# Kernel tuning notes

Hardware: AMD Instinct MI355X
Metric: run time of the kernel (lower is better)

Reference implementation:

```python
import jax, jax.numpy as jnp
import numpy as np
import math

# ---- static configuration (mirrors init_kwargs) ----
NQ = 8            # n_qubits (main register)
NA = 2            # n_ancilla = ceil(log2(n_select))
NSEL = 4          # n_select
DEG = 3           # degree
LAYERS = 2        # n_ansatz_layers
KLOC = 2          # k_local
LATENT = 128
B = 256
NROTS = 4 * NQ * LAYERS          # 64
GROUPS = [(s, s + 1) for s in range(NQ - KLOC + 1)]  # sliding 2-local -> 7 groups
NOBS = len(GROUPS)
KDIM = 2 ** KLOC                  # 4
C64 = jnp.complex64
TWO_PI = 2.0 * math.pi

CNOT = jnp.array([[1, 0, 0, 0], [0, 1, 0, 0], [0, 0, 0, 1], [0, 0, 1, 0]], dtype=C64)

# ---- gate matrices (theta may be traced) ----
def ry_mat(th):
    c = jnp.cos(th / 2).astype(C64); s = jnp.sin(th / 2).astype(C64)
    return jnp.stack([jnp.stack([c, -s]), jnp.stack([s, c])])

def rz_mat(th):
    return jnp.diag(jnp.stack([jnp.exp(-0.5j * th), jnp.exp(0.5j * th)])).astype(C64)

def crx_mat(th):
    c = jnp.cos(th / 2).astype(C64); isn = (-1j * jnp.sin(th / 2)).astype(C64)
    one = jnp.ones((), C64)
    m = jnp.zeros((4, 4), C64)
    m = m.at[0, 0].set(one).at[1, 1].set(one)
    m = m.at[2, 2].set(c).at[3, 3].set(c).at[2, 3].set(isn).at[3, 2].set(isn)
    return m

# ---- state-vector gate application (state: (2,)*rank, wire = axis) ----
def apply_1q(state, U, w):
    return jnp.moveaxis(jnp.tensordot(U, state, axes=((1,), (w,))), 0, w)

def apply_2q(state, U, w0, w1):
    st = jnp.tensordot(U.reshape(2, 2, 2, 2), state, axes=((2, 3), (w0, w1)))
    return jnp.moveaxis(st, (0, 1), (w0, w1))

def _sim14_ops(nq, layers):
    ops, idx = [], 0
    for _ in range(layers):
        for i in range(nq):
            ops.append(("ry", (i,), idx)); idx += 1
        for i in range(nq - 1, -1, -1):
            ops.append(("crx", (i, (i + 1) % nq), idx)); idx += 1
        for i in range(nq):
            ops.append(("ry", (i,), idx)); idx += 1
        for i in [nq - 1] + list(range(nq - 1)):
            ops.append(("crx", (i, (i - 1) % nq), idx)); idx += 1
    return ops

def apply_sim14(state, p, layers, adjoint=False):
    ops = _sim14_ops(NQ, layers)
    seq = list(reversed(ops)) if adjoint else ops
    sgn = -1.0 if adjoint else 1.0
    for kind, ws, idx in seq:
        th = sgn * p[idx]
        if kind == "ry":
            state = apply_1q(state, ry_mat(th), ws[0])
        else:
            state = apply_2q(state, crx_mat(th), ws[0], ws[1])
    return state

def pcphase(state, phi):
    # e^{+i phi} on ancilla=|0..0> subspace (first 2^NQ states in (anc, main) ordering), e^{-i phi} elsewhere
    sr = state.reshape(2 ** NQ, 2 ** NA)
    ph = jnp.where(jnp.arange(2 ** NA) == 0, jnp.exp(1j * phi), jnp.exp(-1j * phi)).astype(C64)
    return (sr * ph[None, :]).reshape(state.shape)

def prepare(state, prep_p, adjoint=False):
    if not adjoint:
        for ly in range(NA):          # n_prep_layers == n_ancilla
            for qi in range(NA):
                state = apply_1q(state, ry_mat(prep_p[ly, qi, 0]), NQ + qi)
                state = apply_1q(state, rz_mat(prep_p[ly, qi, 1]), NQ + qi)
            for i in range(NA - 1):
                state = apply_2q(state, CNOT, NQ + i, NQ + i + 1)
    else:
        for ly in reversed(range(NA)):
            for i in reversed(range(NA - 1)):
                state = apply_2q(state, CNOT, NQ + i, NQ + i + 1)
            for qi in reversed(range(NA)):
                state = apply_1q(state, rz_mat(-prep_p[ly, qi, 1]), NQ + qi)
                state = apply_1q(state, ry_mat(-prep_p[ly, qi, 0]), NQ + qi)
    return state

def select(state, ts, adjoint=False):
    # ancilla wires (NQ, NQ+1) are the trailing axes; flattened index == control value s
    sr = state.reshape((2,) * NQ + (2 ** NA,))
    for s in range(NSEL):
        sub = apply_sim14(sr[..., s], ts[s], LAYERS, adjoint=adjoint)
        sr = sr.at[..., s].set(sub)
    return sr.reshape(state.shape)

def create_hermitian(A, Bp, D, N):
    h = jnp.zeros((N, N), C64)
    count = 0
    for i in range(1, N):
        h = h.at[i - 1, i - 1].set(D[i].astype(C64))
        for j in range(i):
            h = h.at[i, j].set((A[count + j] + 1j * Bp[count + j]).astype(C64))
        count += i
    return h + h.conj().T

def simulate(ts, prep_p, sig, qff, H_all):
    # ts: (NSEL, NROTS) for one batch element
    state = jnp.zeros((2,) * (NQ + NA), C64).at[(0,) * (NQ + NA)].set(1.0)
    state = pcphase(state, sig[0])
    for k in range(DEG):
        state = prepare(state, prep_p)
        state = select(state, ts, adjoint=(k % 2 == 1))
        state = prepare(state, prep_p, adjoint=True)
        state = pcphase(state, sig[k + 1])
    state = apply_sim14(state, qff, 1)
    es = []
    for w, (a, b) in enumerate(GROUPS):
        hpsi = apply_2q(state, H_all[w], a, b)
        es.append(jnp.real(jnp.vdot(state, hpsi)))
    return jnp.stack(es).astype(jnp.float32)  # (NOBS,)

def linear(x, w, b):
    return x @ w.T + b

def sinusoidal_embedding(t, dim):
    half = dim // 2
    freqs = jnp.exp(-math.log(10000.0) * jnp.arange(half, dtype=jnp.float32) / half)
    args = t[:, None] * freqs[None]
    return jnp.concatenate([jnp.cos(args), jnp.sin(args)], axis=-1)

def _forward(z_t, t, te_w1, te_b1, te_w2, te_b2, ip_w1, ip_b1, ip_w2, ip_b2,
             prep_params, signal_angles, qff_params, A_obs, B_obs, D_obs, head_w, head_b):
    t_emb = sinusoidal_embedding(t, LATENT)
    t_emb = linear(jax.nn.silu(linear(t_emb, te_w1, te_b1)), te_w2, te_b2)
    h = jnp.concatenate([z_t, t_emb], axis=-1)
    h = linear(jax.nn.silu(linear(h, ip_w1, ip_b1)), ip_w2, ip_b2)
    ts = jax.nn.sigmoid(h).reshape(z_t.shape[0], NSEL, NROTS) * TWO_PI
    H_all = jax.vmap(lambda a, b, d: create_hermitian(a, b, d, KDIM))(A_obs, B_obs, D_obs)  # (NOBS,4,4)
    expvals = jax.vmap(simulate, in_axes=(0, None, None, None, None))(
        ts, prep_params, signal_angles, qff_params, H_all)  # (B, NOBS)
    return linear(expvals, head_w, head_b)  # (B, LATENT)

def setup_inputs() -> dict:
    key = jax.random.key(0)
    ks = jax.random.split(key, 16)
    def n(k, shape, s=0.05):
        return s * jax.random.normal(k, shape, jnp.float32)
    return {
        "z_t": jax.random.normal(ks[0], (B, LATENT), jnp.float32),
        "t": jax.random.uniform(ks[1], (B,), jnp.float32),
        "te_w1": n(ks[2], (LATENT, LATENT)), "te_b1": jnp.zeros((LATENT,), jnp.float32),
        "te_w2": n(ks[3], (LATENT, LATENT)), "te_b2": jnp.zeros((LATENT,), jnp.float32),
        "ip_w1": n(ks[4], (2 * LATENT, 2 * LATENT)), "ip_b1": jnp.zeros((2 * LATENT,), jnp.float32),
        "ip_w2": n(ks[5], (NSEL * NROTS, 2 * LATENT)), "ip_b2": jnp.zeros((NSEL * NROTS,), jnp.float32),
        "prep_params": 0.1 * jax.random.normal(ks[6], (NA, NA, 2), jnp.float32),
        "signal_angles": 0.1 * jax.random.normal(ks[7], (DEG + 1,), jnp.float32),
        "qff_params": jax.random.uniform(ks[8], (4 * NQ,), jnp.float32),
        "A_obs": 2.0 * jax.random.normal(ks[9], (NOBS, KDIM * (KDIM - 1) // 2), jnp.float32),
        "B_obs": 2.0 * jax.random.normal(ks[10], (NOBS, KDIM * (KDIM - 1) // 2), jnp.float32),
        "D_obs": 2.0 * jax.random.normal(ks[11], (NOBS, KDIM), jnp.float32),
        "head_w": n(ks[12], (LATENT, NOBS)), "head_b": jnp.zeros((LATENT,), jnp.float32),
    }

def reference(z_t, t, te_w1, te_b1, te_w2, te_b2, ip_w1, ip_b1, ip_w2, ip_b2,
              prep_params, signal_angles, qff_params, A_obs, B_obs, D_obs, head_w, head_b):
    return _forward(z_t, t, te_w1, te_b1, te_w2, te_b2, ip_w1, ip_b1, ip_w2, ip_b2,
                    prep_params, signal_angles, qff_params, A_obs, B_obs, D_obs, head_w, head_b)
```

## Files before the change

kernel.cpp:

```cpp
#include <hip/hip_runtime.h>
#include <math.h>

#define NOBS 7
#define TWO_PI_F 6.283185307179586f
#define PI_F 3.14159265358979f


constexpr int REG_MASK(int w)  { return w==6 ? 2 : w==7 ? 1 : 0; }
constexpr int LANE_MASK(int w) { return w<=5 ? (1 << (5-w)) : 0; }

template<int LM>
__device__ __forceinline__ float lane_partner(float x) {
  if constexpr (LM == 1) {
    return __int_as_float(__builtin_amdgcn_mov_dpp(__float_as_int(x), 0xB1, 0xF, 0xF, true));
  } else if constexpr (LM == 2) {
    return __int_as_float(__builtin_amdgcn_mov_dpp(__float_as_int(x), 0x4E, 0xF, 0xF, true));
  } else if constexpr (LM == 4) {
    int a = __builtin_amdgcn_mov_dpp(__float_as_int(x), 0x1B, 0xF, 0xF, true);
    return __int_as_float(__builtin_amdgcn_mov_dpp(a, 0x141, 0xF, 0xF, true));
  } else if constexpr (LM == 8) {
    int a = __builtin_amdgcn_mov_dpp(__float_as_int(x), 0x141, 0xF, 0xF, true);
    return __int_as_float(__builtin_amdgcn_mov_dpp(a, 0x140, 0xF, 0xF, true));
  } else if constexpr (LM == 16) {
#if __has_builtin(__builtin_amdgcn_permlane16_swap)
    unsigned xu = __float_as_uint(x);
    auto r = __builtin_amdgcn_permlane16_swap(xu, xu, false, false);
    return (__uint_as_float(r[0]) + __uint_as_float(r[1])) - x;
#else
    return __shfl_xor(x, 16, 64);
#endif
  } else {
#if __has_builtin(__builtin_amdgcn_permlane32_swap)
    unsigned xu = __float_as_uint(x);
    auto r = __builtin_amdgcn_permlane32_swap(xu, xu, false, false);
    return (__uint_as_float(r[0]) + __uint_as_float(r[1])) - x;
#else
    return __shfl_xor(x, 32, 64);
#endif
  }
}

template<int LM>
__device__ __forceinline__ float xor_sum(float x) {
  if constexpr (LM == 16) {
#if __has_builtin(__builtin_amdgcn_permlane16_swap)
    unsigned xu = __float_as_uint(x);
    auto r = __builtin_amdgcn_permlane16_swap(xu, xu, false, false);
    return __uint_as_float(r[0]) + __uint_as_float(r[1]);
#else
    return x + __shfl_xor(x, 16, 64);
#endif
  } else if constexpr (LM == 32) {
#if __has_builtin(__builtin_amdgcn_permlane32_swap)
    unsigned xu = __float_as_uint(x);
    auto r = __builtin_amdgcn_permlane32_swap(xu, xu, false, false);
    return __uint_as_float(r[0]) + __uint_as_float(r[1]);
#else
    return x + __shfl_xor(x, 32, 64);
#endif
  } else {
    return x + lane_partner<LM>(x);
  }
}

__device__ __forceinline__ float rdlane(float v, int idx) {
  return __int_as_float(__builtin_amdgcn_readlane(__float_as_int(v), idx));
}

__device__ __forceinline__ float2 cmul(float2 a, float2 b) {
  return make_float2(a.x*b.x - a.y*b.y, a.x*b.y + a.y*b.x);
}
__device__ __forceinline__ float2 cmulc(float2 a, float2 b) {
  return make_float2(a.x*b.x + a.y*b.y, a.y*b.x - a.x*b.y);
}
__device__ __forceinline__ float2 cadd(float2 a, float2 b) {
  return make_float2(a.x + b.x, a.y + b.y);
}


template<int W>
__device__ __forceinline__ void ry_gate(float* vr, float* vi, int lane,
                                        float creg, float sreg, int idx, float sg)
{
  float c = rdlane(creg, idx);
  float s = sg * rdlane(sreg, idx);
  if constexpr (REG_MASK(W) != 0) {
    constexpr int m = REG_MASK(W);
#pragma unroll
    for (int r = 0; r < 4; ++r) {
      if (r & m) continue;
      const int r1 = r | m;
      float a0 = vr[r], a1 = vr[r1];
      vr[r]  = c*a0 - s*a1;  vr[r1] = s*a0 + c*a1;
      float b0 = vi[r], b1 = vi[r1];
      vi[r]  = c*b0 - s*b1;  vi[r1] = s*b0 + c*b1;
    }
  } else {
    constexpr int LM = LANE_MASK(W);
    const float ls = (lane & LM) ? s : -s;
#pragma unroll
    for (int r = 0; r < 4; ++r) {
      float pr = lane_partner<LM>(vr[r]);
      float pi = lane_partner<LM>(vi[r]);
      vr[r] = c*vr[r] + ls*pr;
      vi[r] = c*vi[r] + ls*pi;
    }
  }
}

template<int WC, int WT>
__device__ __forceinline__ void crx_gate(float* vr, float* vi, int lane,
                                         float creg, float sreg, int idx, float sg)
{
  float c = rdlane(creg, idx);
  float s = sg * rdlane(sreg, idx);
  constexpr int MC = REG_MASK(WC), LC = LANE_MASK(WC);
  constexpr int MT = REG_MASK(WT), LT = LANE_MASK(WT);
  if constexpr (MC != 0 && MT != 0) {
#pragma unroll
    for (int r = 0; r < 4; ++r) {
      if (!(r & MC) || (r & MT)) continue;
      const int r1 = r | MT;
      float xr = vr[r], xi = vi[r], yr = vr[r1], yi = vi[r1];
      vr[r]  = c*xr + s*yi;  vi[r]  = c*xi - s*yr;
      vr[r1] = c*yr + s*xi;  vi[r1] = c*yi - s*xr;
    }
  } else if constexpr (MC != 0) {
#pragma unroll
    for (int r = 0; r < 4; ++r) {
      if (!(r & MC)) continue;
      float pr = lane_partner<LT>(vr[r]);
      float pi = lane_partner<LT>(vi[r]);
      vr[r] = c*vr[r] + s*pi;
      vi[r] = c*vi[r] - s*pr;
    }
  } else if constexpr (MT != 0) {
    const bool act = (lane & LC) != 0;
#pragma unroll
    for (int r = 0; r < 4; ++r) {
      if (r & MT) continue;
      const int r1 = r | MT;
      float xr = vr[r], xi = vi[r], yr = vr[r1], yi = vi[r1];
      float nxr = c*xr + s*yi, nxi = c*xi - s*yr;
      float nyr = c*yr + s*xi, nyi = c*yi - s*xr;
      vr[r]  = act ? nxr : xr;  vi[r]  = act ? nxi : xi;
      vr[r1] = act ? nyr : yr;  vi[r1] = act ? nyi : yi;
    }
  } else {
    const bool act = (lane & LC) != 0;
#pragma unroll
    for (int r = 0; r < 4; ++r) {
      float pr = lane_partner<LT>(vr[r]);
      float pi = lane_partner<LT>(vi[r]);
      float nr = c*vr[r] + s*pi;
      float ni = c*vi[r] - s*pr;
      vr[r] = act ? nr : vr[r];
      vi[r] = act ? ni : vi[r];
    }
  }
}


__device__ __forceinline__ void sim14_fwd(float* vr, float* vi, int lane,
                                          float ct, float st, int off, float sg)
{
  ry_gate<0>(vr,vi,lane,ct,st,off+0,sg);  ry_gate<1>(vr,vi,lane,ct,st,off+1,sg);
  ry_gate<2>(vr,vi,lane,ct,st,off+2,sg);  ry_gate<3>(vr,vi,lane,ct,st,off+3,sg);
  ry_gate<4>(vr,vi,lane,ct,st,off+4,sg);  ry_gate<5>(vr,vi,lane,ct,st,off+5,sg);
  ry_gate<6>(vr,vi,lane,ct,st,off+6,sg);  ry_gate<7>(vr,vi,lane,ct,st,off+7,sg);
  crx_gate<7,0>(vr,vi,lane,ct,st,off+8,sg);  crx_gate<6,7>(vr,vi,lane,ct,st,off+9,sg);
  crx_gate<5,6>(vr,vi,lane,ct,st,off+10,sg); crx_gate<4,5>(vr,vi,lane,ct,st,off+11,sg);
  crx_gate<3,4>(vr,vi,lane,ct,st,off+12,sg); crx_gate<2,3>(vr,vi,lane,ct,st,off+13,sg);
  crx_gate<1,2>(vr,vi,lane,ct,st,off+14,sg); crx_gate<0,1>(vr,vi,lane,ct,st,off+15,sg);
  ry_gate<0>(vr,vi,lane,ct,st,off+16,sg); ry_gate<1>(vr,vi,lane,ct,st,off+17,sg);
  ry_gate<2>(vr,vi,lane,ct,st,off+18,sg); ry_gate<3>(vr,vi,lane,ct,st,off+19,sg);
  ry_gate<4>(vr,vi,lane,ct,st,off+20,sg); ry_gate<5>(vr,vi,lane,ct,st,off+21,sg);
  ry_gate<6>(vr,vi,lane,ct,st,off+22,sg); ry_gate<7>(vr,vi,lane,ct,st,off+23,sg);
  crx_gate<7,6>(vr,vi,lane,ct,st,off+24,sg); crx_gate<0,7>(vr,vi,lane,ct,st,off+25,sg);
  crx_gate<1,0>(vr,vi,lane,ct,st,off+26,sg); crx_gate<2,1>(vr,vi,lane,ct,st,off+27,sg);
  crx_gate<3,2>(vr,vi,lane,ct,st,off+28,sg); crx_gate<4,3>(vr,vi,lane,ct,st,off+29,sg);
  crx_gate<5,4>(vr,vi,lane,ct,st,off+30,sg); crx_gate<6,5>(vr,vi,lane,ct,st,off+31,sg);
}

__device__ __forceinline__ void sim14_adj(float* vr, float* vi, int lane,
                                          float ct, float st, int off)
{
  const float sg = -1.f;
  crx_gate<6,5>(vr,vi,lane,ct,st,off+31,sg); crx_gate<5,4>(vr,vi,lane,ct,st,off+30,sg);
  crx_gate<4,3>(vr,vi,lane,ct,st,off+29,sg); crx_gate<3,2>(vr,vi,lane,ct,st,off+28,sg);
  crx_gate<2,1>(vr,vi,lane,ct,st,off+27,sg); crx_gate<1,0>(vr,vi,lane,ct,st,off+26,sg);
  crx_gate<0,7>(vr,vi,lane,ct,st,off+25,sg); crx_gate<7,6>(vr,vi,lane,ct,st,off+24,sg);
  ry_gate<7>(vr,vi,lane,ct,st,off+23,sg); ry_gate<6>(vr,vi,lane,ct,st,off+22,sg);
  ry_gate<5>(vr,vi,lane,ct,st,off+21,sg); ry_gate<4>(vr,vi,lane,ct,st,off+20,sg);
  ry_gate<3>(vr,vi,lane,ct,st,off+19,sg); ry_gate<2>(vr,vi,lane,ct,st,off+18,sg);
  ry_gate<1>(vr,vi,lane,ct,st,off+17,sg); ry_gate<0>(vr,vi,lane,ct,st,off+16,sg);
  crx_gate<0,1>(vr,vi,lane,ct,st,off+15,sg); crx_gate<1,2>(vr,vi,lane,ct,st,off+14,sg);
  crx_gate<2,3>(vr,vi,lane,ct,st,off+13,sg); crx_gate<3,4>(vr,vi,lane,ct,st,off+12,sg);
  crx_gate<4,5>(vr,vi,lane,ct,st,off+11,sg); crx_gate<5,6>(vr,vi,lane,ct,st,off+10,sg);
  crx_gate<6,7>(vr,vi,lane,ct,st,off+9,sg);  crx_gate<7,0>(vr,vi,lane,ct,st,off+8,sg);
  ry_gate<7>(vr,vi,lane,ct,st,off+7,sg); ry_gate<6>(vr,vi,lane,ct,st,off+6,sg);
  ry_gate<5>(vr,vi,lane,ct,st,off+5,sg); ry_gate<4>(vr,vi,lane,ct,st,off+4,sg);
  ry_gate<3>(vr,vi,lane,ct,st,off+3,sg); ry_gate<2>(vr,vi,lane,ct,st,off+2,sg);
  ry_gate<1>(vr,vi,lane,ct,st,off+1,sg); ry_gate<0>(vr,vi,lane,ct,st,off+0,sg);
}


template<int IN, int NP, int MODE>
__device__ __forceinline__ void mlp_layer(const float* __restrict__ W,
    const float* __restrict__ bias, const float* xl, float* yl,
    int rbase, int lane)
{
  const int sub = lane & 7;
  const int g   = lane >> 3;
#pragma unroll
  for (int p = 0; p < NP; ++p) {
    const int row = rbase + p * 8 + g;
    const float4* w4 = (const float4*)(W + row * IN) + sub;
    const float4* x4 = (const float4*)xl + sub;
    float acc = 0.f;
#pragma unroll
    for (int it = 0; it < IN / 32; ++it) {
      float4 w = w4[it * 8], e = x4[it * 8];
      acc += w.x*e.x + w.y*e.y + w.z*e.z + w.w*e.w;
    }
    acc = xor_sum<1>(acc);
    acc = xor_sum<2>(acc);
    acc = xor_sum<4>(acc);
    if (sub == 0) {
      float a = acc + bias[row];
      if constexpr (MODE == 0) {
        yl[row] = a / (1.f + __expf(-a));
      } else if constexpr (MODE == 1) {
        yl[row] = a;
      } else {
        float th = PI_F / (1.f + __expf(-a));
        float sn, cn;
        __sincosf(th, &sn, &cn);
        ((float2*)yl)[row] = make_float2(cn, sn);
      }
    }
  }
}


__global__ __launch_bounds__(256) void qsvt_kernel(
    const float* __restrict__ z_t, const float* __restrict__ t,
    const float* __restrict__ te_w1, const float* __restrict__ te_b1,
    const float* __restrict__ te_w2, const float* __restrict__ te_b2,
    const float* __restrict__ ip_w1, const float* __restrict__ ip_b1,
    const float* __restrict__ ip_w2, const float* __restrict__ ip_b2,
    const float* __restrict__ prep_p, const float* __restrict__ sig,
    const float* __restrict__ qff, const float* __restrict__ A_obs,
    const float* __restrict__ B_obs, const float* __restrict__ D_obs,
    const float* __restrict__ head_w, const float* __restrict__ head_b,
    float* __restrict__ out)
{
  __shared__ __align__(16) float emb[128];
  __shared__ __align__(16) float y1[128];
  __shared__ __align__(16) float hbuf[256];
  __shared__ __align__(16) float h1[256];
  __shared__ __align__(16) float2 seltab[256];
  __shared__ __align__(16) float2 qtab[32];
  __shared__ __align__(16) float2 xbuf[64*17];
  __shared__ __align__(16) float dumpR[4][256];
  __shared__ __align__(16) float dumpI[4][256];
  __shared__ float redbuf[NOBS][4];
  __shared__ float hdc[NOBS][3], hxc[NOBS][6], hyc[NOBS][6];
  __shared__ __align__(16) float shw[128*NOBS];
  __shared__ __align__(16) float shb[128];

  const int tid  = threadIdx.x;
  const int lane = tid & 63;
  const int s    = tid >> 6;
  const int b    = blockIdx.x;

  if (tid < 128) {
    int j = tid & 63;
    float fr = __expf(-9.210340371976184f * (float)j / 64.f);
    float arg = t[b] * fr;
    float sn, cn;
    __sincosf(arg, &sn, &cn);
    emb[tid] = (tid < 64) ? cn : sn;
  } else if (tid < 160) {
    int j = tid - 128;
    float sn, cn;
    __sincosf(0.5f * qff[j], &sn, &cn);
    qtab[j] = make_float2(cn, sn);
  }
  __syncthreads();

  mlp_layer<128, 4, 0>(te_w1, te_b1, emb, y1, s * 32, lane);
  if (tid < 128) hbuf[tid] = z_t[b * 128 + tid];
  __syncthreads();

  mlp_layer<128, 4, 1>(te_w2, te_b2, y1, hbuf + 128, s * 32, lane);
  __syncthreads();

  mlp_layer<256, 8, 0>(ip_w1, ip_b1, hbuf, h1, s * 64, lane);
  __syncthreads();

  mlp_layer<256, 8, 2>(ip_w2, ip_b2, h1, (float*)seltab, s * 64, lane);

  if (tid < NOBS * 6)      { hxc[tid/6][tid%6] = A_obs[tid]; hyc[tid/6][tid%6] = B_obs[tid]; }
  else if (tid >= 64 && tid < 64 + NOBS*3) { int q = tid - 64; hdc[q/3][q%3] = 2.f * D_obs[(q/3)*4 + (q%3) + 1]; }
#pragma unroll
  for (int i = tid; i < 128*NOBS; i += 256) shw[i] = head_w[i];
  if (tid < 128) shb[tid] = head_b[tid];

  float2 Ga[2][2][2], Gb[2][2][2];
#pragma unroll
  for (int ly = 0; ly < 2; ++ly) {
#pragma unroll
    for (int qi = 0; qi < 2; ++qi) {
      float y = prep_p[ly*4 + qi*2 + 0], z = prep_p[ly*4 + qi*2 + 1];
      float cy, sy, cz, sz;
      __sincosf(0.5f*y, &sy, &cy);
      __sincosf(0.5f*z, &sz, &cz);
      float2 g00 = make_float2( cy*cz, -cy*sz);
      float2 g01 = make_float2(-sy*cz,  sy*sz);
      float2 g10 = make_float2( sy*cz,  sy*sz);
      float2 g11 = make_float2( cy*cz,  cy*sz);
      if (qi == 0) { Ga[ly][0][0]=g00; Ga[ly][0][1]=g01; Ga[ly][1][0]=g10; Ga[ly][1][1]=g11; }
      else         { Gb[ly][0][0]=g00; Gb[ly][0][1]=g01; Gb[ly][1][0]=g10; Gb[ly][1][1]=g11; }
    }
  }
  float2 M[2][4][4];
#pragma unroll
  for (int ly = 0; ly < 2; ++ly) {
    float2 T[4][4];
#pragma unroll
    for (int i = 0; i < 4; ++i)
#pragma unroll
      for (int j = 0; j < 4; ++j)
        T[i][j] = cmul(Ga[ly][i>>1][j>>1], Gb[ly][i&1][j&1]);
#pragma unroll
    for (int j = 0; j < 4; ++j) {
      M[ly][0][j] = T[0][j]; M[ly][1][j] = T[1][j];
      M[ly][2][j] = T[3][j]; M[ly][3][j] = T[2][j];
    }
  }
  float2 U[4][4];
#pragma unroll
  for (int i = 0; i < 4; ++i)
#pragma unroll
    for (int j = 0; j < 4; ++j) {
      float2 acc = make_float2(0.f, 0.f);
#pragma unroll
      for (int kk = 0; kk < 4; ++kk) acc = cadd(acc, cmul(M[1][i][kk], M[0][kk][j]));
      U[i][j] = acc;
    }
  float2 Urow[4], Ucol[4];
#pragma unroll
  for (int j = 0; j < 4; ++j) {
    Urow[j] = s==0 ? U[0][j] : s==1 ? U[1][j] : s==2 ? U[2][j] : U[3][j];
    Ucol[j] = s==0 ? U[j][0] : s==1 ? U[j][1] : s==2 ? U[j][2] : U[j][3];
  }
  float sg0 = sig[0], sg1 = sig[1], sg2 = sig[2], sg3 = sig[3];
  float c1, s1v, c2, s2v, c3, s3v;
  __sincosf(sg1, &s1v, &c1);
  __sincosf(sg2, &s2v, &c2);
  __sincosf(sg3, &s3v, &c3);
  float2 R1[4], R2[4], RF[4];
  {
    float s3s = (s == 0) ? s3v : -s3v;
    float2 d3 = make_float2(c3, s3s);
#pragma unroll
    for (int sp = 0; sp < 4; ++sp) {
      float2 a1 = make_float2(0.f, 0.f), a2 = make_float2(0.f, 0.f);
#pragma unroll
      for (int j = 0; j < 4; ++j) {
        float2 uspj = sp==0 ? U[0][j] : sp==1 ? U[1][j] : sp==2 ? U[2][j] : U[3][j];
        float2 tt = cmulc(Urow[j], uspj);
        float sj = (j == 0) ? 1.f : -1.f;
        a1 = cadd(a1, cmul(tt, make_float2(c1, sj*s1v)));
        a2 = cadd(a2, cmul(tt, make_float2(c2, sj*s2v)));
      }
      R1[sp] = a1; R2[sp] = a2;
      RF[sp] = cmul(d3, make_float2(Ucol[sp].x, -Ucol[sp].y));
    }
  }
  __syncthreads();

  float2 mycs = seltab[(s << 6) | lane];
  float selc = mycs.x, sels = mycs.y;
  float2 myq = qtab[lane & 31];
  float qc = myq.x, qs = myq.y;

  float vr[4], vi[4];
  {
    float s0n, c0n;
    __sincosf(sg0, &s0n, &c0n);
    float2 a0 = cmul(Urow[0], make_float2(c0n, s0n));
#pragma unroll
    for (int r = 0; r < 4; ++r) { vr[r] = 0.f; vi[r] = 0.f; }
    if (lane == 0) { vr[0] = a0.x; vi[0] = a0.y; }
  }

  sim14_fwd(vr, vi, lane, selc, sels, 0, 1.f);
  sim14_fwd(vr, vi, lane, selc, sels, 32, 1.f);
  {
#pragma unroll
    for (int r = 0; r < 4; ++r) xbuf[lane*17 + r*4 + s] = make_float2(vr[r], vi[r]);
    __syncthreads();
#pragma unroll
    for (int r = 0; r < 4; ++r) {
      const float2* p = &xbuf[lane*17 + r*4];
      float2 o = cmul(R1[0], p[0]);
      o = cadd(o, cmul(R1[1], p[1]));
      o = cadd(o, cmul(R1[2], p[2]));
      o = cadd(o, cmul(R1[3], p[3]));
      vr[r] = o.x; vi[r] = o.y;
    }
    __syncthreads();
  }
  sim14_adj(vr, vi, lane, selc, sels, 32);
  sim14_adj(vr, vi, lane, selc, sels, 0);
  {
#pragma unroll
    for (int r = 0; r < 4; ++r) xbuf[lane*17 + r*4 + s] = make_float2(vr[r], vi[r]);
    __syncthreads();
#pragma unroll
    for (int r = 0; r < 4; ++r) {
      const float2* p = &xbuf[lane*17 + r*4];
      float2 o = cmul(R2[0], p[0]);
      o = cadd(o, cmul(R2[1], p[1]));
      o = cadd(o, cmul(R2[2], p[2]));
      o = cadd(o, cmul(R2[3], p[3]));
      vr[r] = o.x; vi[r] = o.y;
    }
    __syncthreads();
  }
  sim14_fwd(vr, vi, lane, selc, sels, 0, 1.f);
  sim14_fwd(vr, vi, lane, selc, sels, 32, 1.f);
  {
#pragma unroll
    for (int r = 0; r < 4; ++r) xbuf[lane*17 + r*4 + s] = make_float2(vr[r], vi[r]);
    __syncthreads();
#pragma unroll
    for (int r = 0; r < 4; ++r) {
      const float2* p = &xbuf[lane*17 + r*4];
      float2 o = cmul(RF[0], p[0]);
      o = cadd(o, cmul(RF[1], p[1]));
      o = cadd(o, cmul(RF[2], p[2]));
      o = cadd(o, cmul(RF[3], p[3]));
      vr[r] = o.x; vi[r] = o.y;
    }
    __syncthreads();
  }
  sim14_fwd(vr, vi, lane, qc, qs, 0, 1.f);

  *(float4*)&dumpR[s][lane*4] = make_float4(vr[0], vr[1], vr[2], vr[3]);
  *(float4*)&dumpI[s][lane*4] = make_float4(vi[0], vi[1], vi[2], vi[3]);

#pragma unroll
  for (int w = 0; w < NOBS; ++w) {
    const int pb = 6 - w;
    int g = lane;
    int ib = ((g >> pb) << (pb + 2)) | (g & ((1 << pb) - 1));
    float xr[4], xi[4];
#pragma unroll
    for (int i = 0; i < 4; ++i) { xr[i] = dumpR[s][ib + (i << pb)]; xi[i] = dumpI[s][ib + (i << pb)]; }
    float a = hdc[w][0] * (xr[0]*xr[0] + xi[0]*xi[0])
            + hdc[w][1] * (xr[1]*xr[1] + xi[1]*xi[1])
            + hdc[w][2] * (xr[2]*xr[2] + xi[2]*xi[2]);
    const int oi[6] = {1, 2, 2, 3, 3, 3};
    const int oj[6] = {0, 0, 1, 0, 1, 2};
#pragma unroll
    for (int k2 = 0; k2 < 6; ++k2) {
      int i = oi[k2], j = oj[k2];
      float rr = xr[i]*xr[j] + xi[i]*xi[j];
      float ii = xr[i]*xi[j] - xi[i]*xr[j];
      a += 2.f * (hxc[w][k2]*rr - hyc[w][k2]*ii);
    }
    a = xor_sum<32>(a);
    a = xor_sum<16>(a);
    a = xor_sum<8>(a);
    a = xor_sum<4>(a);
    a = xor_sum<2>(a);
    a = xor_sum<1>(a);
    if (lane == 0) redbuf[w][s] = a;
  }
  __syncthreads();

  if (tid < 128) {
    float acc = shb[tid];
#pragma unroll
    for (int w = 0; w < NOBS; ++w) {
      float ev = redbuf[w][0] + redbuf[w][1] + redbuf[w][2] + redbuf[w][3];
      acc += ev * shw[tid*NOBS + w];
    }
    out[b * 128 + tid] = acc;
  }
}

extern "C" void kernel_launch(void* const* d_in, const int* in_sizes, int n_in,
                              void* d_out, int out_size, void* d_ws, size_t ws_size,
                              hipStream_t stream) {
  (void)n_in; (void)out_size; (void)d_ws; (void)ws_size;
  const float* z_t    = (const float*)d_in[0];
  const float* t      = (const float*)d_in[1];
  const float* te_w1  = (const float*)d_in[2];
  const float* te_b1  = (const float*)d_in[3];
  const float* te_w2  = (const float*)d_in[4];
  const float* te_b2  = (const float*)d_in[5];
  const float* ip_w1  = (const float*)d_in[6];
  const float* ip_b1  = (const float*)d_in[7];
  const float* ip_w2  = (const float*)d_in[8];
  const float* ip_b2  = (const float*)d_in[9];
  const float* prep_p = (const float*)d_in[10];
  const float* sig    = (const float*)d_in[11];
  const float* qff    = (const float*)d_in[12];
  const float* A_obs  = (const float*)d_in[13];
  const float* B_obs  = (const float*)d_in[14];
  const float* D_obs  = (const float*)d_in[15];
  const float* head_w = (const float*)d_in[16];
  const float* head_b = (const float*)d_in[17];
  float* out = (float*)d_out;

  int B = in_sizes[1];
  qsvt_kernel<<<B, 256, 0, stream>>>(
      z_t, t, te_w1, te_b1, te_w2, te_b2, ip_w1, ip_b1, ip_w2, ip_b2,
      prep_p, sig, qff, A_obs, B_obs, D_obs, head_w, head_b, out);
}
```

Baseline: 128.8 us.

## Split state vector across two wave halves with LDS exchange for wire 6

Doubles the block to 512 threads so each ancilla branch's 256-amplitude state is spread over two wavefronts, each lane holding 2 amplitudes instead of 4. Wire 6 now spans the two wave halves, so gates acting on it exchange data through a double-buffered shared-memory buffer with a block barrier. The MLP stages and the observable loop are re-partitioned across the 8 waves. This halves per-thread gate work and register use, but adds many __syncthreads on the critical gate chain.

New measurement: 127.2 us. About the same (-1.2%).

```diff
diff --git a/kernel.cpp b/kernel.cpp
--- a/kernel.cpp
+++ b/kernel.cpp
@@ -2,12 +2,8 @@
 #include <math.h>
 
 #define NOBS 7
-#define TWO_PI_F 6.283185307179586f
 #define PI_F 3.14159265358979f
 
-
-constexpr int REG_MASK(int w)  { return w==6 ? 2 : w==7 ? 1 : 0; }
-constexpr int LANE_MASK(int w) { return w<=5 ? (1 << (5-w)) : 0; }
 
 template<int LM>
 __device__ __forceinline__ float lane_partner(float x) {
@@ -77,131 +73,180 @@
   return make_float2(a.x + b.x, a.y + b.y);
 }
 
+struct Ctx {
+  float4* xw;
+  int pp;
+  int wv, lane, h;
+};
+
+__device__ __forceinline__ float4 wexch(Ctx& cx, const float* vr, const float* vi) {
+  float4* buf = cx.xw + cx.pp * 512;
+  buf[cx.wv * 64 + cx.lane] = make_float4(vr[0], vr[1], vi[0], vi[1]);
+  __syncthreads();
+  float4 p = buf[(cx.wv ^ 4) * 64 + cx.lane];
+  cx.pp ^= 1;
+  return p;
+}
+
 
 template<int W>
-__device__ __forceinline__ void ry_gate(float* vr, float* vi, int lane,
-                                        float creg, float sreg, int idx, float sg)
-{
-  float c = rdlane(creg, idx);
-  float s = sg * rdlane(sreg, idx);
-  if constexpr (REG_MASK(W) != 0) {
-    constexpr int m = REG_MASK(W);
-#pragma unroll
-    for (int r = 0; r < 4; ++r) {
-      if (r & m) continue;
-      const int r1 = r | m;
-      float a0 = vr[r], a1 = vr[r1];
-      vr[r]  = c*a0 - s*a1;  vr[r1] = s*a0 + c*a1;
-      float b0 = vi[r], b1 = vi[r1];
-      vi[r]  = c*b0 - s*b1;  vi[r1] = s*b0 + c*b1;
-    }
-  } else {
-    constexpr int LM = LANE_MASK(W);
-    const float ls = (lane & LM) ? s : -s;
-#pragma unroll
-    for (int r = 0; r < 4; ++r) {
-      float pr = lane_partner<LM>(vr[r]);
-      float pi = lane_partner<LM>(vi[r]);
-      vr[r] = c*vr[r] + ls*pr;
-      vi[r] = c*vi[r] + ls*pi;
-    }
-  }
-}
-
-template<int WC, int WT>
-__device__ __forceinline__ void crx_gate(float* vr, float* vi, int lane,
-                                         float creg, float sreg, int idx, float sg)
-{
-  float c = rdlane(creg, idx);
-  float s = sg * rdlane(sreg, idx);
-  constexpr int MC = REG_MASK(WC), LC = LANE_MASK(WC);
-  constexpr int MT = REG_MASK(WT), LT = LANE_MASK(WT);
-  if constexpr (MC != 0 && MT != 0) {
-#pragma unroll
-    for (int r = 0; r < 4; ++r) {
-      if (!(r & MC) || (r & MT)) continue;
-      const int r1 = r | MT;
-      float xr = vr[r], xi = vi[r], yr = vr[r1], yi = vi[r1];
-      vr[r]  = c*xr + s*yi;  vi[r]  = c*xi - s*yr;
-      vr[r1] = c*yr + s*xi;  vi[r1] = c*yi - s*xr;
-    }
-  } else if constexpr (MC != 0) {
-#pragma unroll
-    for (int r = 0; r < 4; ++r) {
-      if (!(r & MC)) continue;
+__device__ __forceinline__ void ry_lane(float* vr, float* vi, Ctx& cx,
+                                        float ct, float st, int idx, float sg) {
+  float c = rdlane(ct, idx), s = sg * rdlane(st, idx);
+  constexpr int LM = 1 << (5 - W);
+  const float ls = (cx.lane & LM) ? s : -s;
+#pragma unroll
+  for (int r = 0; r < 2; ++r) {
+    float pr = lane_partner<LM>(vr[r]);
+    float pi = lane_partner<LM>(vi[r]);
+    vr[r] = c*vr[r] + ls*pr;
+    vi[r] = c*vi[r] + ls*pi;
+  }
+}
+
+__device__ __forceinline__ void ry_wave6(float* vr, float* vi, Ctx& cx,
+                                         float ct, float st, int idx, float sg) {
+  float c = rdlane(ct, idx), s = sg * rdlane(st, idx);
+  float4 P = wexch(cx, vr, vi);
+  const float ls = cx.h ? s : -s;
+  vr[0] = c*vr[0] + ls*P.x;  vr[1] = c*vr[1] + ls*P.y;
+  vi[0] = c*vi[0] + ls*P.z;  vi[1] = c*vi[1] + ls*P.w;
+}
+
+__device__ __forceinline__ void ry_reg7(float* vr, float* vi,
+                                        float ct, float st, int idx, float sg) {
+  float c = rdlane(ct, idx), s = sg * rdlane(st, idx);
+  float a0 = vr[0], a1 = vr[1];
+  vr[0] = c*a0 - s*a1;  vr[1] = s*a0 + c*a1;
+  float b0 = vi[0], b1 = vi[1];
+  vi[0] = c*b0 - s*b1;  vi[1] = s*b0 + c*b1;
+}
+
+template<int C, int T>
+__device__ __forceinline__ void crx_ll(float* vr, float* vi, Ctx& cx,
+                                       float ct, float st, int idx, float sg) {
+  float c = rdlane(ct, idx), s = sg * rdlane(st, idx);
+  constexpr int LC = 1 << (5 - C), LT = 1 << (5 - T);
+  const bool act = (cx.lane & LC) != 0;
+  const float cp = act ? c : 1.f, sp = act ? s : 0.f;
+#pragma unroll
+  for (int r = 0; r < 2; ++r) {
+    float pr = lane_partner<LT>(vr[r]);
+    float pi = lane_partner<LT>(vi[r]);
+    vr[r] = cp*vr[r] + sp*pi;
+    vi[r] = cp*vi[r] - sp*pr;
+  }
+}
+
+template<int T>
+__device__ __forceinline__ void crx_7l(float* vr, float* vi, Ctx& cx,
+                                       float ct, float st, int idx, float sg) {
+  float c = rdlane(ct, idx), s = sg * rdlane(st, idx);
+  constexpr int LT = 1 << (5 - T);
+  float pr = lane_partner<LT>(vr[1]);
+  float pi = lane_partner<LT>(vi[1]);
+  vr[1] = c*vr[1] + s*pi;
+  vi[1] = c*vi[1] - s*pr;
+}
+
+template<int C>
+__device__ __forceinline__ void crx_l7(float* vr, float* vi, Ctx& cx,
+                                       float ct, float st, int idx, float sg) {
+  float c = rdlane(ct, idx), s = sg * rdlane(st, idx);
+  constexpr int LC = 1 << (5 - C);
+  const bool act = (cx.lane & LC) != 0;
+  const float cp = act ? c : 1.f, sp = act ? s : 0.f;
+  float xr = vr[0], xi = vi[0], yr = vr[1], yi = vi[1];
+  vr[0] = cp*xr + sp*yi;  vi[0] = cp*xi - sp*yr;
+  vr[1] = cp*yr + sp*xi;  vi[1] = cp*yi - sp*xr;
+}
+
+template<int C>
+__device__ __forceinline__ void crx_l6(float* vr, float* vi, Ctx& cx,
+                                       float ct, float st, int idx, float sg) {
+  float c = rdlane(ct, idx), s = sg * rdlane(st, idx);
+  float4 P = wexch(cx, vr, vi);
+  constexpr int LC = 1 << (5 - C);
+  const bool act = (cx.lane & LC) != 0;
+  const float cp = act ? c : 1.f, sp = act ? s : 0.f;
+  vr[0] = cp*vr[0] + sp*P.z;  vi[0] = cp*vi[0] - sp*P.x;
+  vr[1] = cp*vr[1] + sp*P.w;  vi[1] = cp*vi[1] - sp*P.y;
+}
+
+__device__ __forceinline__ void crx_76(float* vr, float* vi, Ctx& cx,
+                                       float ct, float st, int idx, float sg) {
+  float c = rdlane(ct, idx), s = sg * rdlane(st, idx);
+  float4 P = wexch(cx, vr, vi);
+  vr[1] = c*vr[1] + s*P.w;
+  vi[1] = c*vi[1] - s*P.y;
+}
+
+__device__ __forceinline__ void crx_67(float* vr, float* vi, Ctx& cx,
+                                       float ct, float st, int idx, float sg) {
+  if (cx.h) {
+    float c = rdlane(ct, idx), s = sg * rdlane(st, idx);
+    float xr = vr[0], xi = vi[0], yr = vr[1], yi = vi[1];
+    vr[0] = c*xr + s*yi;  vi[0] = c*xi - s*yr;
+    vr[1] = c*yr + s*xi;  vi[1] = c*yi - s*xr;
+  }
+}
+
+template<int T>
+__device__ __forceinline__ void crx_6l(float* vr, float* vi, Ctx& cx,
+                                       float ct, float st, int idx, float sg) {
+  if (cx.h) {
+    float c = rdlane(ct, idx), s = sg * rdlane(st, idx);
+    constexpr int LT = 1 << (5 - T);
+#pragma unroll
+    for (int r = 0; r < 2; ++r) {
       float pr = lane_partner<LT>(vr[r]);
       float pi = lane_partner<LT>(vi[r]);
       vr[r] = c*vr[r] + s*pi;
       vi[r] = c*vi[r] - s*pr;
     }
-  } else if constexpr (MT != 0) {
-    const bool act = (lane & LC) != 0;
-#pragma unroll
-    for (int r = 0; r < 4; ++r) {
-      if (r & MT) continue;
-      const int r1 = r | MT;
-      float xr = vr[r], xi = vi[r], yr = vr[r1], yi = vi[r1];
-      float nxr = c*xr + s*yi, nxi = c*xi - s*yr;
-      float nyr = c*yr + s*xi, nyi = c*yi - s*xr;
-      vr[r]  = act ? nxr : xr;  vi[r]  = act ? nxi : xi;
-      vr[r1] = act ? nyr : yr;  vi[r1] = act ? nyi : yi;
-    }
-  } else {
-    const bool act = (lane & LC) != 0;
-#pragma unroll
-    for (int r = 0; r < 4; ++r) {
-      float pr = lane_partner<LT>(vr[r]);
-      float pi = lane_partner<LT>(vi[r]);
-      float nr = c*vr[r] + s*pi;
-      float ni = c*vi[r] - s*pr;
-      vr[r] = act ? nr : vr[r];
-      vi[r] = act ? ni : vi[r];
-    }
-  }
-}
-
-
-__device__ __forceinline__ void sim14_fwd(float* vr, float* vi, int lane,
-                                          float ct, float st, int off, float sg)
-{
-  ry_gate<0>(vr,vi,lane,ct,st,off+0,sg);  ry_gate<1>(vr,vi,lane,ct,st,off+1,sg);
-  ry_gate<2>(vr,vi,lane,ct,st,off+2,sg);  ry_gate<3>(vr,vi,lane,ct,st,off+3,sg);
-  ry_gate<4>(vr,vi,lane,ct,st,off+4,sg);  ry_gate<5>(vr,vi,lane,ct,st,off+5,sg);
-  ry_gate<6>(vr,vi,lane,ct,st,off+6,sg);  ry_gate<7>(vr,vi,lane,ct,st,off+7,sg);
-  crx_gate<7,0>(vr,vi,lane,ct,st,off+8,sg);  crx_gate<6,7>(vr,vi,lane,ct,st,off+9,sg);
-  crx_gate<5,6>(vr,vi,lane,ct,st,off+10,sg); crx_gate<4,5>(vr,vi,lane,ct,st,off+11,sg);
-  crx_gate<3,4>(vr,vi,lane,ct,st,off+12,sg); crx_gate<2,3>(vr,vi,lane,ct,st,off+13,sg);
-  crx_gate<1,2>(vr,vi,lane,ct,st,off+14,sg); crx_gate<0,1>(vr,vi,lane,ct,st,off+15,sg);
-  ry_gate<0>(vr,vi,lane,ct,st,off+16,sg); ry_gate<1>(vr,vi,lane,ct,st,off+17,sg);
-  ry_gate<2>(vr,vi,lane,ct,st,off+18,sg); ry_gate<3>(vr,vi,lane,ct,st,off+19,sg);
-  ry_gate<4>(vr,vi,lane,ct,st,off+20,sg); ry_gate<5>(vr,vi,lane,ct,st,off+21,sg);
-  ry_gate<6>(vr,vi,lane,ct,st,off+22,sg); ry_gate<7>(vr,vi,lane,ct,st,off+23,sg);
-  crx_gate<7,6>(vr,vi,lane,ct,st,off+24,sg); crx_gate<0,7>(vr,vi,lane,ct,st,off+25,sg);
-  crx_gate<1,0>(vr,vi,lane,ct,st,off+26,sg); crx_gate<2,1>(vr,vi,lane,ct,st,off+27,sg);
-  crx_gate<3,2>(vr,vi,lane,ct,st,off+28,sg); crx_gate<4,3>(vr,vi,lane,ct,st,off+29,sg);
-  crx_gate<5,4>(vr,vi,lane,ct,st,off+30,sg); crx_gate<6,5>(vr,vi,lane,ct,st,off+31,sg);
-}
-
-__device__ __forceinline__ void sim14_adj(float* vr, float* vi, int lane,
-                                          float ct, float st, int off)
-{
+  }
+}
+
+
+__device__ __forceinline__ void sim14_fwd(float* vr, float* vi, Ctx& cx,
+                                          float ct, float st, int off, float sg) {
+  ry_lane<0>(vr,vi,cx,ct,st,off+0,sg); ry_lane<1>(vr,vi,cx,ct,st,off+1,sg);
+  ry_lane<2>(vr,vi,cx,ct,st,off+2,sg); ry_lane<3>(vr,vi,cx,ct,st,off+3,sg);
+  ry_lane<4>(vr,vi,cx,ct,st,off+4,sg); ry_lane<5>(vr,vi,cx,ct,st,off+5,sg);
+  ry_wave6(vr,vi,cx,ct,st,off+6,sg);   ry_reg7(vr,vi,ct,st,off+7,sg);
+  crx_7l<0>(vr,vi,cx,ct,st,off+8,sg);  crx_67(vr,vi,cx,ct,st,off+9,sg);
+  crx_l6<5>(vr,vi,cx,ct,st,off+10,sg); crx_ll<4,5>(vr,vi,cx,ct,st,off+11,sg);
+  crx_ll<3,4>(vr,vi,cx,ct,st,off+12,sg); crx_ll<2,3>(vr,vi,cx,ct,st,off+13,sg);
+  crx_ll<1,2>(vr,vi,cx,ct,st,off+14,sg); crx_ll<0,1>(vr,vi,cx,ct,st,off+15,sg);
+  ry_lane<0>(vr,vi,cx,ct,st,off+16,sg); ry_lane<1>(vr,vi,cx,ct,st,off+17,sg);
+  ry_lane<2>(vr,vi,cx,ct,st,off+18,sg); ry_lane<3>(vr,vi,cx,ct,st,off+19,sg);
+  ry_lane<4>(vr,vi,cx,ct,st,off+20,sg); ry_lane<5>(vr,vi,cx,ct,st,off+21,sg);
+  ry_wave6(vr,vi,cx,ct,st,off+22,sg);   ry_reg7(vr,vi,ct,st,off+23,sg);
+  crx_76(vr,vi,cx,ct,st,off+24,sg);     crx_l7<0>(vr,vi,cx,ct,st,off+25,sg);
+  crx_ll<1,0>(vr,vi,cx,ct,st,off+26,sg); crx_ll<2,1>(vr,vi,cx,ct,st,off+27,sg);
+  crx_ll<3,2>(vr,vi,cx,ct,st,off+28,sg); crx_ll<4,3>(vr,vi,cx,ct,st,off+29,sg);
+  crx_ll<5,4>(vr,vi,cx,ct,st,off+30,sg); crx_6l<5>(vr,vi,cx,ct,st,off+31,sg);
+}
+
+__device__ __forceinline__ void sim14_adj(float* vr, float* vi, Ctx& cx,
+                                          float ct, float st, int off) {
   const float sg = -1.f;
-  crx_gate<6,5>(vr,vi,lane,ct,st,off+31,sg); crx_gate<5,4>(vr,vi,lane,ct,st,off+30,sg);
-  crx_gate<4,3>(vr,vi,lane,ct,st,off+29,sg); crx_gate<3,2>(vr,vi,lane,ct,st,off+28,sg);
-  crx_gate<2,1>(vr,vi,lane,ct,st,off+27,sg); crx_gate<1,0>(vr,vi,lane,ct,st,off+26,sg);
-  crx_gate<0,7>(vr,vi,lane,ct,st,off+25,sg); crx_gate<7,6>(vr,vi,lane,ct,st,off+24,sg);
-  ry_gate<7>(vr,vi,lane,ct,st,off+23,sg); ry_gate<6>(vr,vi,lane,ct,st,off+22,sg);
-  ry_gate<5>(vr,vi,lane,ct,st,off+21,sg); ry_gate<4>(vr,vi,lane,ct,st,off+20,sg);
-  ry_gate<3>(vr,vi,lane,ct,st,off+19,sg); ry_gate<2>(vr,vi,lane,ct,st,off+18,sg);
-  ry_gate<1>(vr,vi,lane,ct,st,off+17,sg); ry_gate<0>(vr,vi,lane,ct,st,off+16,sg);
-  crx_gate<0,1>(vr,vi,lane,ct,st,off+15,sg); crx_gate<1,2>(vr,vi,lane,ct,st,off+14,sg);
-  crx_gate<2,3>(vr,vi,lane,ct,st,off+13,sg); crx_gate<3,4>(vr,vi,lane,ct,st,off+12,sg);
-  crx_gate<4,5>(vr,vi,lane,ct,st,off+11,sg); crx_gate<5,6>(vr,vi,lane,ct,st,off+10,sg);
-  crx_gate<6,7>(vr,vi,lane,ct,st,off+9,sg);  crx_gate<7,0>(vr,vi,lane,ct,st,off+8,sg);
-  ry_gate<7>(vr,vi,lane,ct,st,off+7,sg); ry_gate<6>(vr,vi,lane,ct,st,off+6,sg);
-  ry_gate<5>(vr,vi,lane,ct,st,off+5,sg); ry_gate<4>(vr,vi,lane,ct,st,off+4,sg);
-  ry_gate<3>(vr,vi,lane,ct,st,off+3,sg); ry_gate<2>(vr,vi,lane,ct,st,off+2,sg);
-  ry_gate<1>(vr,vi,lane,ct,st,off+1,sg); ry_gate<0>(vr,vi,lane,ct,st,off+0,sg);
+  crx_6l<5>(vr,vi,cx,ct,st,off+31,sg); crx_ll<5,4>(vr,vi,cx,ct,st,off+30,sg);
+  crx_ll<4,3>(vr,vi,cx,ct,st,off+29,sg); crx_ll<3,2>(vr,vi,cx,ct,st,off+28,sg);
+  crx_ll<2,1>(vr,vi,cx,ct,st,off+27,sg); crx_ll<1,0>(vr,vi,cx,ct,st,off+26,sg);
+  crx_l7<0>(vr,vi,cx,ct,st,off+25,sg);   crx_76(vr,vi,cx,ct,st,off+24,sg);
+  ry_reg7(vr,vi,ct,st,off+23,sg);        ry_wave6(vr,vi,cx,ct,st,off+22,sg);
+  ry_lane<5>(vr,vi,cx,ct,st,off+21,sg); ry_lane<4>(vr,vi,cx,ct,st,off+20,sg);
+  ry_lane<3>(vr,vi,cx,ct,st,off+19,sg); ry_lane<2>(vr,vi,cx,ct,st,off+18,sg);
+  ry_lane<1>(vr,vi,cx,ct,st,off+17,sg); ry_lane<0>(vr,vi,cx,ct,st,off+16,sg);
+  crx_ll<0,1>(vr,vi,cx,ct,st,off+15,sg); crx_ll<1,2>(vr,vi,cx,ct,st,off+14,sg);
+  crx_ll<2,3>(vr,vi,cx,ct,st,off+13,sg); crx_ll<3,4>(vr,vi,cx,ct,st,off+12,sg);
+  crx_ll<4,5>(vr,vi,cx,ct,st,off+11,sg); crx_l6<5>(vr,vi,cx,ct,st,off+10,sg);
+  crx_67(vr,vi,cx,ct,st,off+9,sg);       crx_7l<0>(vr,vi,cx,ct,st,off+8,sg);
+  ry_reg7(vr,vi,ct,st,off+7,sg);         ry_wave6(vr,vi,cx,ct,st,off+6,sg);
+  ry_lane<5>(vr,vi,cx,ct,st,off+5,sg); ry_lane<4>(vr,vi,cx,ct,st,off+4,sg);
+  ry_lane<3>(vr,vi,cx,ct,st,off+3,sg); ry_lane<2>(vr,vi,cx,ct,st,off+2,sg);
+  ry_lane<1>(vr,vi,cx,ct,st,off+1,sg); ry_lane<0>(vr,vi,cx,ct,st,off+0,sg);
 }
 
 
@@ -243,7 +288,7 @@
 }
 
 
-__global__ __launch_bounds__(256) void qsvt_kernel(
+__global__ __launch_bounds__(512) void qsvt_kernel(
     const float* __restrict__ z_t, const float* __restrict__ t,
     const float* __restrict__ te_w1, const float* __restrict__ te_b1,
     const float* __restrict__ te_w2, const float* __restrict__ te_b2,
@@ -261,17 +306,20 @@
   __shared__ __align__(16) float h1[256];
   __shared__ __align__(16) float2 seltab[256];
   __shared__ __align__(16) float2 qtab[32];
-  __shared__ __align__(16) float2 xbuf[64*17];
+  __shared__ __align__(16) float4 xw[2 * 8 * 64];
+  __shared__ __align__(16) float2 xanc[128 * 9];
   __shared__ __align__(16) float dumpR[4][256];
   __shared__ __align__(16) float dumpI[4][256];
   __shared__ float redbuf[NOBS][4];
   __shared__ float hdc[NOBS][3], hxc[NOBS][6], hyc[NOBS][6];
-  __shared__ __align__(16) float shw[128*NOBS];
+  __shared__ __align__(16) float shw[128 * NOBS];
   __shared__ __align__(16) float shb[128];
 
   const int tid  = threadIdx.x;
   const int lane = tid & 63;
-  const int s    = tid >> 6;
+  const int wv   = tid >> 6;
+  const int s    = wv & 3;
+  const int h    = wv >> 2;
   const int b    = blockIdx.x;
 
   if (tid < 128) {
@@ -289,22 +337,22 @@
   }
   __syncthreads();
 
-  mlp_layer<128, 4, 0>(te_w1, te_b1, emb, y1, s * 32, lane);
+  mlp_layer<128, 2, 0>(te_w1, te_b1, emb, y1, wv * 16, lane);
   if (tid < 128) hbuf[tid] = z_t[b * 128 + tid];
   __syncthreads();
 
-  mlp_layer<128, 4, 1>(te_w2, te_b2, y1, hbuf + 128, s * 32, lane);
-  __syncthreads();
-
-  mlp_layer<256, 8, 0>(ip_w1, ip_b1, hbuf, h1, s * 64, lane);
-  __syncthreads();
-
-  mlp_layer<256, 8, 2>(ip_w2, ip_b2, h1, (float*)seltab, s * 64, lane);
+  mlp_layer<128, 2, 1>(te_w2, te_b2, y1, hbuf + 128, wv * 16, lane);
+  __syncthreads();
+
+  mlp_layer<256, 4, 0>(ip_w1, ip_b1, hbuf, h1, wv * 32, lane);
+  __syncthreads();
+
+  mlp_layer<256, 4, 2>(ip_w2, ip_b2, h1, (float*)seltab, wv * 32, lane);
 
   if (tid < NOBS * 6)      { hxc[tid/6][tid%6] = A_obs[tid]; hyc[tid/6][tid%6] = B_obs[tid]; }
   else if (tid >= 64 && tid < 64 + NOBS*3) { int q = tid - 64; hdc[q/3][q%3] = 2.f * D_obs[(q/3)*4 + (q%3) + 1]; }
 #pragma unroll
-  for (int i = tid; i < 128*NOBS; i += 256) shw[i] = head_w[i];
+  for (int i = tid; i < 128*NOBS; i += 512) shw[i] = head_w[i];
   if (tid < 128) shb[tid] = head_b[tid];
 
   float2 Ga[2][2][2], Gb[2][2][2];
@@ -386,25 +434,28 @@
   float2 myq = qtab[lane & 31];
   float qc = myq.x, qs = myq.y;
 
-  float vr[4], vi[4];
-  {
+  Ctx cx; cx.xw = xw; cx.pp = 0; cx.wv = wv; cx.lane = lane; cx.h = h;
+
+  float vr[2], vi[2];
+  vr[0] = 0.f; vr[1] = 0.f; vi[0] = 0.f; vi[1] = 0.f;
+  if (lane == 0 && h == 0) {
     float s0n, c0n;
     __sincosf(sg0, &s0n, &c0n);
     float2 a0 = cmul(Urow[0], make_float2(c0n, s0n));
-#pragma unroll
-    for (int r = 0; r < 4; ++r) { vr[r] = 0.f; vi[r] = 0.f; }
-    if (lane == 0) { vr[0] = a0.x; vi[0] = a0.y; }
-  }
-
-  sim14_fwd(vr, vi, lane, selc, sels, 0, 1.f);
-  sim14_fwd(vr, vi, lane, selc, sels, 32, 1.f);
+    vr[0] = a0.x; vi[0] = a0.y;
+  }
+
+  const int ancbase = (h * 64 + lane) * 9;
+
+  sim14_fwd(vr, vi, cx, selc, sels, 0, 1.f);
+  sim14_fwd(vr, vi, cx, selc, sels, 32, 1.f);
   {
 #pragma unroll
-    for (int r = 0; r < 4; ++r) xbuf[lane*17 + r*4 + s] = make_float2(vr[r], vi[r]);
+    for (int r = 0; r < 2; ++r) xanc[ancbase + r*4 + s] = make_float2(vr[r], vi[r]);
     __syncthreads();
 #pragma unroll
-    for (int r = 0; r < 4; ++r) {
-      const float2* p = &xbuf[lane*17 + r*4];
+    for (int r = 0; r < 2; ++r) {
+      const float2* p = &xanc[ancbase + r*4];
       float2 o = cmul(R1[0], p[0]);
       o = cadd(o, cmul(R1[1], p[1]));
       o = cadd(o, cmul(R1[2], p[2]));
@@ -413,15 +464,15 @@
     }
     __syncthreads();
   }
-  sim14_adj(vr, vi, lane, selc, sels, 32);
-  sim14_adj(vr, vi, lane, selc, sels, 0);
+  sim14_adj(vr, vi, cx, selc, sels, 32);
+  sim14_adj(vr, vi, cx, selc, sels, 0);
   {
 #pragma unroll
-    for (int r = 0; r < 4; ++r) xbuf[lane*17 + r*4 + s] = make_float2(vr[r], vi[r]);
+    for (int r = 0; r < 2; ++r) xanc[ancbase + r*4 + s] = make_float2(vr[r], vi[r]);
     __syncthreads();
 #pragma unroll
-    for (int r = 0; r < 4; ++r) {
-      const float2* p = &xbuf[lane*17 + r*4];
+    for (int r = 0; r < 2; ++r) {
+      const float2* p = &xanc[ancbase + r*4];
       float2 o = cmul(R2[0], p[0]);
       o = cadd(o, cmul(R2[1], p[1]));
       o = cadd(o, cmul(R2[2], p[2]));
@@ -430,15 +481,15 @@
     }
     __syncthreads();
   }
-  sim14_fwd(vr, vi, lane, selc, sels, 0, 1.f);
-  sim14_fwd(vr, vi, lane, selc, sels, 32, 1.f);
+  sim14_fwd(vr, vi, cx, selc, sels, 0, 1.f);
+  sim14_fwd(vr, vi, cx, selc, sels, 32, 1.f);
   {
 #pragma unroll
-    for (int r = 0; r < 4; ++r) xbuf[lane*17 + r*4 + s] = make_float2(vr[r], vi[r]);
+    for (int r = 0; r < 2; ++r) xanc[ancbase + r*4 + s] = make_float2(vr[r], vi[r]);
     __syncthreads();
 #pragma unroll
-    for (int r = 0; r < 4; ++r) {
-      const float2* p = &xbuf[lane*17 + r*4];
+    for (int r = 0; r < 2; ++r) {
+      const float2* p = &xanc[ancbase + r*4];
       float2 o = cmul(RF[0], p[0]);
       o = cadd(o, cmul(RF[1], p[1]));
       o = cadd(o, cmul(RF[2], p[2]));
@@ -447,13 +498,14 @@
     }
     __syncthreads();
   }
-  sim14_fwd(vr, vi, lane, qc, qs, 0, 1.f);
-
-  *(float4*)&dumpR[s][lane*4] = make_float4(vr[0], vr[1], vr[2], vr[3]);
-  *(float4*)&dumpI[s][lane*4] = make_float4(vi[0], vi[1], vi[2], vi[3]);
-
-#pragma unroll
-  for (int w = 0; w < NOBS; ++w) {
+  sim14_fwd(vr, vi, cx, qc, qs, 0, 1.f);
+
+  *(float2*)&dumpR[s][(lane << 2) | (h << 1)] = make_float2(vr[0], vr[1]);
+  *(float2*)&dumpI[s][(lane << 2) | (h << 1)] = make_float2(vi[0], vi[1]);
+  __syncthreads();
+
+  const int w0 = h ? 4 : 0, w1 = h ? NOBS : 4;
+  for (int w = w0; w < w1; ++w) {
     const int pb = 6 - w;
     int g = lane;
     int ib = ((g >> pb) << (pb + 2)) | (g & ((1 << pb) - 1));
@@ -518,7 +570,7 @@
   float* out = (float*)d_out;
 
   int B = in_sizes[1];
-  qsvt_kernel<<<B, 256, 0, stream>>>(
+  qsvt_kernel<<<B, 512, 0, stream>>>(
       z_t, t, te_w1, te_b1, te_w2, te_b2, ip_w1, ip_b1, ip_w2, ip_b2,
       prep_p, sig, qff, A_obs, B_obs, D_obs, head_w, head_b, out);
 }
```
